# Kernel tuning notes

Hardware: AMD Instinct MI355X
Metric: run time of the kernel (lower is better)

The kernel has to match this reference:

```python
import jax, jax.numpy as jnp
import numpy as np
from jax import lax

# IVF+PQ search (FAISS IVF1024,PQ8x8 with nprobe=32, by_residual=False variant):
# 1) coarse quantizer: L2 distance of each query to nlist centroids, keep top nprobe lists
# 2) ADC: per-query LUT of squared distances between query subvectors and PQ codebooks,
#    database distance = sum over subquantizers of LUT gathered at the stored codes
# 3) mask database vectors whose IVF list was not probed, return indices of top_k smallest

NPROBE = 32  # top_n_centroids
BIG = jnp.float32(1e30)


def setup_inputs() -> dict:
    key = jax.random.key(0)
    ks = jax.random.split(key, 5)
    Q, D = 256, 128
    M, K = 8, 256          # pq_subvecs, 2**pq_nbits
    dsub = D // M          # 16
    nlist = 1024
    N = 250_000            # database size
    queries = jax.random.normal(ks[0], (Q, D), dtype=jnp.float32)
    centroids = jax.random.normal(ks[1], (nlist, D), dtype=jnp.float32)
    codebooks = jax.random.normal(ks[2], (M, K, dsub), dtype=jnp.float32)
    db_codes = jax.random.randint(ks[3], (N, M), 0, K, dtype=jnp.int32)
    db_list = jax.random.randint(ks[4], (N,), 0, nlist, dtype=jnp.int32)
    return {"queries": queries, "centroids": centroids, "codebooks": codebooks,
            "db_codes": db_codes, "db_list": db_list, "top_k": 100}


def _masked_adc_distances(queries, centroids, codebooks, db_codes, db_list):
    Q, D = queries.shape
    nlist = centroids.shape[0]
    M, K, dsub = codebooks.shape
    # ---- coarse quantizer: ||q - c||^2 over [Q, nlist] ----
    coarse = (jnp.sum(queries * queries, -1, keepdims=True)
              + jnp.sum(centroids * centroids, -1)[None, :]
              - 2.0 * queries @ centroids.T)
    _, probed = lax.top_k(-coarse, NPROBE)                      # [Q, NPROBE] list ids
    probe_mask = jnp.zeros((Q, nlist), dtype=bool).at[
        jnp.arange(Q)[:, None], probed].set(True)               # [Q, nlist]
    allowed = probe_mask[:, db_list]                            # [Q, N]
    # ---- PQ ADC lookup table: ||q_sub - codeword||^2, [Q, M, K] ----
    qs = queries.reshape(Q, M, dsub)
    lut = (jnp.sum(qs * qs, -1)[:, :, None]
           + jnp.sum(codebooks * codebooks, -1)[None, :, :]
           - 2.0 * jnp.einsum('qmd,mkd->qmk', qs, codebooks))   # [Q, M, K]
    # ---- accumulate gathered LUT entries over subquantizers ----
    dist = lut[:, 0, db_codes[:, 0]]                            # [Q, N]
    for m in range(1, M):
        dist = dist + lut[:, m, db_codes[:, m]]
    return jnp.where(allowed, dist, BIG)


def reference(queries, centroids, codebooks, db_codes, db_list, top_k):
    dist = _masked_adc_distances(queries, centroids, codebooks, db_codes, db_list)
    _, indices = lax.top_k(-dist, top_k)                        # smallest distances
    return indices
```

## Files before the change

### kernel.cpp

```cpp
#include <hip/hip_runtime.h>

#define DDIM 128
#define MSUB 8
#define KCODE 256
#define DSUB 16
#define NLIST 1024
#define NPROBE 32
#define TOPK 100
#define HBINS 4096
#define COLL_CAP 2048
#define RCAP 10
#define SCHUNK 1024


__device__ __forceinline__ float xla_sumsq128(const float* x) {
  float s[16];
  #pragma unroll
  for (int j = 0; j < 16; ++j) {
    float p0 = __fmul_rn(x[j],       x[j]);
    float p1 = __fmul_rn(x[j + 16],  x[j + 16]);
    float p2 = __fmul_rn(x[j + 32],  x[j + 32]);
    float p3 = __fmul_rn(x[j + 48],  x[j + 48]);
    float p4 = __fmul_rn(x[j + 64],  x[j + 64]);
    float p5 = __fmul_rn(x[j + 80],  x[j + 80]);
    float p6 = __fmul_rn(x[j + 96],  x[j + 96]);
    float p7 = __fmul_rn(x[j + 112], x[j + 112]);
    float r0 = __fadd_rn(p0, p4);
    float r1 = __fadd_rn(p1, p5);
    float r2 = __fadd_rn(p2, p6);
    float r3 = __fadd_rn(p3, p7);
    s[j] = __fadd_rn(__fadd_rn(r0, r1), __fadd_rn(r2, r3));
  }
  float a[8], b[4], c[2];
  #pragma unroll
  for (int j = 0; j < 8; ++j) a[j] = __fadd_rn(s[j], s[j + 8]);
  #pragma unroll
  for (int j = 0; j < 4; ++j) b[j] = __fadd_rn(a[j], a[j + 4]);
  #pragma unroll
  for (int j = 0; j < 2; ++j) c[j] = __fadd_rn(b[j], b[j + 2]);
  return __fadd_rn(c[0], c[1]);
}

__device__ __forceinline__ float xla_sumsq16(const float* x) {
  float p[16];
  #pragma unroll
  for (int j = 0; j < 16; ++j) p[j] = __fmul_rn(x[j], x[j]);
  float s8[8], s4[4], s2[2];
  #pragma unroll
  for (int j = 0; j < 8; ++j) s8[j] = __fadd_rn(p[j], p[j + 8]);
  #pragma unroll
  for (int j = 0; j < 4; ++j) s4[j] = __fadd_rn(s8[j], s8[j + 4]);
  #pragma unroll
  for (int j = 0; j < 2; ++j) s2[j] = __fadd_rn(s4[j], s4[j + 2]);
  return __fadd_rn(s2[0], s2[1]);
}

__device__ __forceinline__ float chain_dot16(const float* a, const float* b) {
  float dot = 0.f;
  #pragma unroll
  for (int d = 0; d < DSUB; ++d) dot = __fmaf_rn(a[d], b[d], dot);
  return dot;
}

__device__ __forceinline__ float adc_dist(const float* lut, unsigned long long code) {
  float d = lut[(unsigned)(code & 255ULL)];
  d = __fadd_rn(d, lut[256  + (unsigned)((code >> 8)  & 255ULL)]);
  d = __fadd_rn(d, lut[512  + (unsigned)((code >> 16) & 255ULL)]);
  d = __fadd_rn(d, lut[768  + (unsigned)((code >> 24) & 255ULL)]);
  d = __fadd_rn(d, lut[1024 + (unsigned)((code >> 32) & 255ULL)]);
  d = __fadd_rn(d, lut[1280 + (unsigned)((code >> 40) & 255ULL)]);
  d = __fadd_rn(d, lut[1536 + (unsigned)((code >> 48) & 255ULL)]);
  d = __fadd_rn(d, lut[1792 + (unsigned)((code >> 56) & 255ULL)]);
  return d;
}

__device__ __forceinline__ unsigned block_scan_incl(unsigned v, volatile unsigned* wsum,
                                                    int t, int nwaves) {
  int lane = t & 63, wid = t >> 6;
  #pragma unroll
  for (int off = 1; off < 64; off <<= 1) {
    unsigned u = __shfl_up(v, off, 64);
    if (lane >= off) v += u;
  }
  if (lane == 63) wsum[wid] = v;
  __syncthreads();
  if (wid == 0 && lane < nwaves) {
    unsigned wv = wsum[lane];
    #pragma unroll
    for (int off = 1; off < 16; off <<= 1) {
      unsigned u = __shfl_up(wv, off, 64);
      if (lane >= off) wv += u;
    }
    wsum[lane] = wv;
  }
  __syncthreads();
  return v + (wid > 0 ? wsum[wid - 1] : 0u);
}

__global__ __launch_bounds__(256) void k_coarse(const float* __restrict__ queries,
                                                const float* __restrict__ centroids,
                                                unsigned long long* __restrict__ keys_g) {
  const int qi = blockIdx.x >> 2;
  const int part = blockIdx.x & 3;
  const int t = threadIdx.x;
  __shared__ float qs[DDIM];
  if (t < DDIM) qs[t] = queries[qi * DDIM + t];
  __syncthreads();
  const float qq = xla_sumsq128(qs);
  const int c = part * 256 + t;
  const float* cr = centroids + (size_t)c * DDIM;
  float cbuf[DDIM];
  #pragma unroll
  for (int d = 0; d < DDIM; d += 4) {
    float4 cv = *(const float4*)(cr + d);
    cbuf[d] = cv.x; cbuf[d + 1] = cv.y; cbuf[d + 2] = cv.z; cbuf[d + 3] = cv.w;
  }
  const float cc = xla_sumsq128(cbuf);
  float dot = 0.f;
  #pragma unroll
  for (int d = 0; d < DDIM; ++d) dot = __fmaf_rn(qs[d], cbuf[d], dot);
  float dist = __fsub_rn(__fadd_rn(qq, cc), __fmul_rn(2.0f, dot));
  unsigned bits = __float_as_uint(dist);
  keys_g[(size_t)qi * NLIST + c] = ((unsigned long long)bits << 32) | (unsigned)c;
}

__global__ __launch_bounds__(256) void k_lut(const float* __restrict__ queries,
                                             const float* __restrict__ codebooks,
                                             const int* __restrict__ db_list, int N,
                                             float* __restrict__ lut_g,
                                             unsigned* __restrict__ counts) {
  const int qi = blockIdx.x;
  const int t = threadIdx.x;
  __shared__ float qs[DDIM];
  __shared__ unsigned hist[NLIST];
  if (t < DDIM) qs[t] = queries[qi * DDIM + t];
  for (int i = t; i < NLIST; i += 256) hist[i] = 0;
  __syncthreads();

  for (int j = 0; j < MSUB; ++j) {
    int idx = j * KCODE + t;
    const float* cb = codebooks + (size_t)idx * DSUB;
    const float* qsub = qs + j * DSUB;
    float cbv[DSUB], qv[DSUB];
    #pragma unroll
    for (int d = 0; d < DSUB; ++d) { cbv[d] = cb[d]; qv[d] = qsub[d]; }
    const float qq16 = xla_sumsq16(qv);
    const float cc16 = xla_sumsq16(cbv);
    const float dot16 = chain_dot16(qv, cbv);
    lut_g[(size_t)qi * (MSUB * KCODE) + idx] =
        __fsub_rn(__fadd_rn(qq16, cc16), __fmul_rn(2.0f, dot16));
  }

  for (int n = qi * 256 + t; n < N; n += 256 * 256)
    atomicAdd(&hist[db_list[n]], 1u);
  __syncthreads();
  for (int i = t; i < NLIST; i += 256)
    if (hist[i]) atomicAdd(&counts[i], hist[i]);
}

__global__ __launch_bounds__(256) void k_scatter(const int* __restrict__ db_list,
                                                 const int* __restrict__ db_codes, int N,
                                                 const unsigned* __restrict__ counts,
                                                 unsigned* __restrict__ cursor,
                                                 int4* __restrict__ pack) {
  __shared__ unsigned lhist[NLIST], lbase[NLIST], sbstart[NLIST];
  __shared__ unsigned wsum[16];
  const int t = threadIdx.x;
  const int base = blockIdx.x * SCHUNK;
  {
    unsigned c0 = counts[t * 4], c1 = counts[t * 4 + 1],
             c2 = counts[t * 4 + 2], c3 = counts[t * 4 + 3];
    unsigned sum4 = c0 + c1 + c2 + c3;
    unsigned incl = block_scan_incl(sum4, wsum, t, 4);
    unsigned excl = incl - sum4;
    sbstart[t * 4] = excl;
    sbstart[t * 4 + 1] = excl + c0;
    sbstart[t * 4 + 2] = excl + c0 + c1;
    sbstart[t * 4 + 3] = excl + c0 + c1 + c2;
  }
  for (int i = t; i < NLIST; i += 256) lhist[i] = 0;
  __syncthreads();
  #pragma unroll
  for (int k = 0; k < SCHUNK / 256; ++k) {
    int n = base + k * 256 + t;
    if (n < N) atomicAdd(&lhist[db_list[n]], 1u);
  }
  __syncthreads();
  for (int i = t; i < NLIST; i += 256) {
    unsigned cnt = lhist[i];
    if (cnt) lbase[i] = sbstart[i] + atomicAdd(&cursor[i], cnt);
    lhist[i] = 0;
  }
  __syncthreads();
  #pragma unroll
  for (int k = 0; k < SCHUNK / 256; ++k) {
    int n = base + k * 256 + t;
    if (n < N) {
      int l = db_list[n];
      unsigned pos = lbase[l] + atomicAdd(&lhist[l], 1u);
      const int4* cp = (const int4*)(db_codes + (size_t)n * MSUB);
      int4 c0 = cp[0], c1 = cp[1];
      unsigned lo = (unsigned)(c0.x & 255) | ((unsigned)(c0.y & 255) << 8) |
                    ((unsigned)(c0.z & 255) << 16) | ((unsigned)(c0.w & 255) << 24);
      unsigned hi = (unsigned)(c1.x & 255) | ((unsigned)(c1.y & 255) << 8) |
                    ((unsigned)(c1.z & 255) << 16) | ((unsigned)(c1.w & 255) << 24);
      pack[pos] = make_int4((int)lo, (int)hi, n, 0);
    }
  }
}

__global__ __launch_bounds__(1024, 1) void k_search(const float* __restrict__ lut_g,
                                                    const unsigned long long* __restrict__ keys_g,
                                                    const unsigned* __restrict__ counts,
                                                    const int4* __restrict__ pack,
                                                    int* __restrict__ out) {
  const int qi = blockIdx.x;
  const int t = threadIdx.x;
  __shared__ float lut_s[MSUB * KCODE];
  __shared__ unsigned hist[HBINS];
  __shared__ unsigned long long coll[COLL_CAP];
  __shared__ unsigned bst[NLIST + 1];
  __shared__ unsigned pstart[NPROBE], pcum[NPROBE + 1];
  __shared__ unsigned wsum[16];
  __shared__ unsigned scnt;
  __shared__ int sT;

  for (int i = t; i < MSUB * KCODE; i += 1024) lut_s[i] = lut_g[(size_t)qi * (MSUB * KCODE) + i];
  const unsigned long long ckey = keys_g[(size_t)qi * NLIST + t];
  for (int i = t; i < HBINS; i += 1024) hist[i] = 0;
  if (t == 0) { scnt = 0; sT = HBINS - 1; }
  {
    unsigned v = counts[t];
    unsigned incl = block_scan_incl(v, wsum, t, 16);
    bst[t + 1] = incl;
    if (t == 0) bst[0] = 0;
  }
  __syncthreads();

  atomicAdd(&hist[(unsigned)(ckey >> 51)], 1u);
  __syncthreads();
  {
    unsigned mysum = 0;
    #pragma unroll
    for (int i = 0; i < 4; ++i) mysum += hist[t * 4 + i];
    unsigned incl = block_scan_incl(mysum, wsum, t, 16);
    unsigned excl = incl - mysum;
    if (excl < NPROBE && NPROBE <= incl) {
      unsigned c2 = excl;
      #pragma unroll
      for (int i = 0; i < 4; ++i) {
        unsigned h = hist[t * 4 + i];
        if (c2 + h >= NPROBE) { sT = t * 4 + i; break; }
        c2 += h;
      }
    }
  }
  __syncthreads();
  {
    const int T32 = sT;
    if ((int)(ckey >> 51) <= T32) {
      unsigned p = atomicAdd(&scnt, 1u);
      if (p < 512) coll[p] = ckey;
    }
  }
  __syncthreads();
  {
    unsigned cnt = scnt; if (cnt > 512) cnt = 512;
    for (unsigned i = t; i < cnt; i += 1024) {
      unsigned long long k2 = coll[i];
      unsigned r = 0;
      for (unsigned j = 0; j < cnt; ++j) r += (coll[j] < k2) ? 1u : 0u;
      if (r < NPROBE) {
        unsigned l = (unsigned)(k2 & 0xffffffffULL);
        pstart[r] = bst[l];
        pcum[r + 1] = bst[l + 1] - bst[l];
      }
    }
  }
  __syncthreads();
  for (int i = t; i < HBINS; i += 1024) hist[i] = 0;
  if (t == 0) {
    scnt = 0; sT = HBINS - 1;
    unsigned acc = 0;
    pcum[0] = 0;
    for (int j = 1; j <= NPROBE; ++j) { acc += pcum[j]; pcum[j] = acc; }
  }
  __syncthreads();
  const unsigned total = pcum[NPROBE];

  unsigned regbits[RCAP], regaddr[RCAP];
  {
    int s = 0;
    for (unsigned g = t; g < total; g += 1024, ++s) {
      int lo = 0, hi = NPROBE;
      while (hi - lo > 1) { int mid = (lo + hi) >> 1; if (pcum[mid] <= g) lo = mid; else hi = mid; }
      unsigned addr = pstart[lo] + (g - pcum[lo]);
      int4 w = pack[addr];
      unsigned long long code = (unsigned)w.x | ((unsigned long long)(unsigned)w.y << 32);
      unsigned bits = __float_as_uint(adc_dist(lut_s, code));
      if (s < RCAP) { regbits[s] = bits; regaddr[s] = addr; }
      atomicAdd(&hist[bits >> 19], 1u);
    }
  }
  __syncthreads();

  {
    unsigned mysum = 0;
    #pragma unroll
    for (int i = 0; i < 4; ++i) mysum += hist[t * 4 + i];
    unsigned incl = block_scan_incl(mysum, wsum, t, 16);
    unsigned excl = incl - mysum;
    if (excl < TOPK && TOPK <= incl) {
      unsigned c = excl;
      #pragma unroll
      for (int i = 0; i < 4; ++i) {
        unsigned h = hist[t * 4 + i];
        if (c + h >= TOPK) { sT = t * 4 + i; break; }
        c += h;
      }
    }
  }
  __syncthreads();
  const int T = sT;

  {
    int s = 0;
    for (unsigned g = t; g < total; g += 1024, ++s) {
      unsigned bits, addr;
      if (s < RCAP) { bits = regbits[s]; addr = regaddr[s]; }
      else {
        int l2 = 0, hi = NPROBE;
        while (hi - l2 > 1) { int mid = (l2 + hi) >> 1; if (pcum[mid] <= g) l2 = mid; else hi = mid; }
        addr = pstart[l2] + (g - pcum[l2]);
        int4 w = pack[addr];
        unsigned long long code = (unsigned)w.x | ((unsigned long long)(unsigned)w.y << 32);
        bits = __float_as_uint(adc_dist(lut_s, code));
      }
      if ((int)(bits >> 19) <= T) {
        unsigned n = (unsigned)pack[addr].z;
        unsigned p = atomicAdd(&scnt, 1u);
        if (p < COLL_CAP) coll[p] = ((unsigned long long)bits << 32) | n;
      }
    }
  }
  __syncthreads();

  unsigned cnt = scnt;
  if (cnt > COLL_CAP) cnt = COLL_CAP;
  for (unsigned i = t; i < cnt; i += 1024) {
    unsigned long long key = coll[i];
    unsigned r = 0;
    for (unsigned j = 0; j < cnt; ++j) r += (coll[j] < key) ? 1u : 0u;
    if (r < TOPK) out[qi * TOPK + r] = (int)(key & 0xffffffffULL);
  }
}

extern "C" void kernel_launch(void* const* d_in, const int* in_sizes, int n_in,
                              void* d_out, int out_size, void* d_ws, size_t ws_size,
                              hipStream_t stream) {
  const float* queries   = (const float*)d_in[0];
  const float* centroids = (const float*)d_in[1];
  const float* codebooks = (const float*)d_in[2];
  const int*   db_codes  = (const int*)d_in[3];
  const int*   db_list   = (const int*)d_in[4];
  const int N = in_sizes[4];
  const int Q = in_sizes[0] / DDIM;
  int* out = (int*)d_out;

  char* p = (char*)d_ws;
  float* lut_g = (float*)p;                         p += (size_t)Q * MSUB * KCODE * 4;
  unsigned long long* keys_g = (unsigned long long*)p; p += (size_t)Q * NLIST * 8;
  unsigned* counts = (unsigned*)p;                  p += NLIST * 4;
  unsigned* cursor = (unsigned*)p;                  p += NLIST * 4;
  int4* pack = (int4*)p;                            p += (size_t)N * 16;

  hipMemsetAsync(counts, 0, (size_t)NLIST * 4 * 2, stream);

  k_coarse<<<Q * 4, 256, 0, stream>>>(queries, centroids, keys_g);
  k_lut<<<Q, 256, 0, stream>>>(queries, codebooks, db_list, N, lut_g, counts);
  k_scatter<<<(N + SCHUNK - 1) / SCHUNK, 256, 0, stream>>>(db_list, db_codes, N,
                                                           counts, cursor, pack);
  k_search<<<Q, 1024, 0, stream>>>(lut_g, keys_g, counts, pack, out);
}
```

Measured before the change: 132.7 us.

## Fuse coarse quantizer and LUT build into search kernel with 512-thread blocks

Coarse centroid distances and the PQ lookup table are now computed per query inside the search kernel, straight into shared memory. This removes the global round trips for keys and LUT and two kernel launches, leaving a small standalone histogram kernel. The search block drops to 512 threads with two blocks per CU, replaces per-element binary searches over probe offsets with a monotone linear walk, and caches packed keys (distance plus index) in registers (RCAP 18). The cost is that each block redoes 1024 centroid dot products serially, and register pressure is higher.

```diff
diff --git a/kernel.cpp b/kernel.cpp
--- a/kernel.cpp
+++ b/kernel.cpp
@@ -9,8 +9,9 @@
 #define TOPK 100
 #define HBINS 4096
 #define COLL_CAP 2048
-#define RCAP 10
+#define RCAP 18
 #define SCHUNK 1024
+#define FTHREADS 512
 
 
 __device__ __forceinline__ float xla_sumsq128(const float* x) {
@@ -97,61 +98,13 @@
   return v + (wid > 0 ? wsum[wid - 1] : 0u);
 }
 
-__global__ __launch_bounds__(256) void k_coarse(const float* __restrict__ queries,
-                                                const float* __restrict__ centroids,
-                                                unsigned long long* __restrict__ keys_g) {
-  const int qi = blockIdx.x >> 2;
-  const int part = blockIdx.x & 3;
+__global__ __launch_bounds__(256) void k_hist(const int* __restrict__ db_list, int N,
+                                              unsigned* __restrict__ counts) {
+  __shared__ unsigned hist[NLIST];
   const int t = threadIdx.x;
-  __shared__ float qs[DDIM];
-  if (t < DDIM) qs[t] = queries[qi * DDIM + t];
-  __syncthreads();
-  const float qq = xla_sumsq128(qs);
-  const int c = part * 256 + t;
-  const float* cr = centroids + (size_t)c * DDIM;
-  float cbuf[DDIM];
-  #pragma unroll
-  for (int d = 0; d < DDIM; d += 4) {
-    float4 cv = *(const float4*)(cr + d);
-    cbuf[d] = cv.x; cbuf[d + 1] = cv.y; cbuf[d + 2] = cv.z; cbuf[d + 3] = cv.w;
-  }
-  const float cc = xla_sumsq128(cbuf);
-  float dot = 0.f;
-  #pragma unroll
-  for (int d = 0; d < DDIM; ++d) dot = __fmaf_rn(qs[d], cbuf[d], dot);
-  float dist = __fsub_rn(__fadd_rn(qq, cc), __fmul_rn(2.0f, dot));
-  unsigned bits = __float_as_uint(dist);
-  keys_g[(size_t)qi * NLIST + c] = ((unsigned long long)bits << 32) | (unsigned)c;
-}
-
-__global__ __launch_bounds__(256) void k_lut(const float* __restrict__ queries,
-                                             const float* __restrict__ codebooks,
-                                             const int* __restrict__ db_list, int N,
-                                             float* __restrict__ lut_g,
-                                             unsigned* __restrict__ counts) {
-  const int qi = blockIdx.x;
-  const int t = threadIdx.x;
-  __shared__ float qs[DDIM];
-  __shared__ unsigned hist[NLIST];
-  if (t < DDIM) qs[t] = queries[qi * DDIM + t];
   for (int i = t; i < NLIST; i += 256) hist[i] = 0;
   __syncthreads();
-
-  for (int j = 0; j < MSUB; ++j) {
-    int idx = j * KCODE + t;
-    const float* cb = codebooks + (size_t)idx * DSUB;
-    const float* qsub = qs + j * DSUB;
-    float cbv[DSUB], qv[DSUB];
-    #pragma unroll
-    for (int d = 0; d < DSUB; ++d) { cbv[d] = cb[d]; qv[d] = qsub[d]; }
-    const float qq16 = xla_sumsq16(qv);
-    const float cc16 = xla_sumsq16(cbv);
-    const float dot16 = chain_dot16(qv, cbv);
-    lut_g[(size_t)qi * (MSUB * KCODE) + idx] =
-        __fsub_rn(__fadd_rn(qq16, cc16), __fmul_rn(2.0f, dot16));
-  }
-
-  for (int n = qi * 256 + t; n < N; n += 256 * 256)
+  for (int n = blockIdx.x * 256 + t; n < N; n += 256 * 256)
     atomicAdd(&hist[db_list[n]], 1u);
   __syncthreads();
   for (int i = t; i < NLIST; i += 256)
@@ -209,14 +162,17 @@
   }
 }
 
-__global__ __launch_bounds__(1024, 1) void k_search(const float* __restrict__ lut_g,
-                                                    const unsigned long long* __restrict__ keys_g,
-                                                    const unsigned* __restrict__ counts,
-                                                    const int4* __restrict__ pack,
-                                                    int* __restrict__ out) {
+__global__ __launch_bounds__(FTHREADS, 2) void k_fused(const float* __restrict__ queries,
+                                                       const float* __restrict__ centroids,
+                                                       const float* __restrict__ codebooks,
+                                                       const unsigned* __restrict__ counts,
+                                                       const int4* __restrict__ pack,
+                                                       int* __restrict__ out) {
   const int qi = blockIdx.x;
   const int t = threadIdx.x;
+  __shared__ float qs[DDIM];
   __shared__ float lut_s[MSUB * KCODE];
+  __shared__ unsigned long long keys_s[NLIST];
   __shared__ unsigned hist[HBINS];
   __shared__ unsigned long long coll[COLL_CAP];
   __shared__ unsigned bst[NLIST + 1];
@@ -225,32 +181,69 @@
   __shared__ unsigned scnt;
   __shared__ int sT;
 
-  for (int i = t; i < MSUB * KCODE; i += 1024) lut_s[i] = lut_g[(size_t)qi * (MSUB * KCODE) + i];
-  const unsigned long long ckey = keys_g[(size_t)qi * NLIST + t];
-  for (int i = t; i < HBINS; i += 1024) hist[i] = 0;
+  if (t < DDIM) qs[t] = queries[qi * DDIM + t];
+  for (int i = t; i < HBINS; i += FTHREADS) hist[i] = 0;
   if (t == 0) { scnt = 0; sT = HBINS - 1; }
-  {
-    unsigned v = counts[t];
-    unsigned incl = block_scan_incl(v, wsum, t, 16);
-    bst[t + 1] = incl;
+  __syncthreads();
+
+  const float qq = xla_sumsq128(qs);
+  #pragma unroll 1
+  for (int rep = 0; rep < 2; ++rep) {
+    const int c = rep * FTHREADS + t;
+    const float* cr = centroids + (size_t)c * DDIM;
+    float cbuf[DDIM];
+    #pragma unroll
+    for (int d = 0; d < DDIM; d += 4) {
+      float4 cv = *(const float4*)(cr + d);
+      cbuf[d] = cv.x; cbuf[d + 1] = cv.y; cbuf[d + 2] = cv.z; cbuf[d + 3] = cv.w;
+    }
+    const float cc = xla_sumsq128(cbuf);
+    float dot = 0.f;
+    #pragma unroll
+    for (int d = 0; d < DDIM; ++d) dot = __fmaf_rn(qs[d], cbuf[d], dot);
+    float dist = __fsub_rn(__fadd_rn(qq, cc), __fmul_rn(2.0f, dot));
+    unsigned bits = __float_as_uint(dist);
+    keys_s[c] = ((unsigned long long)bits << 32) | (unsigned)c;
+    atomicAdd(&hist[bits >> 19], 1u);
+  }
+
+  #pragma unroll 1
+  for (int j = 0; j < (MSUB * KCODE) / FTHREADS; ++j) {
+    int idx = j * FTHREADS + t;
+    const float* cb = codebooks + (size_t)idx * DSUB;
+    const float* qsub = qs + (idx >> 8) * DSUB;
+    float cbv[DSUB], qv[DSUB];
+    #pragma unroll
+    for (int d = 0; d < DSUB; ++d) { cbv[d] = cb[d]; qv[d] = qsub[d]; }
+    const float qq16 = xla_sumsq16(qv);
+    const float cc16 = xla_sumsq16(cbv);
+    const float dot16 = chain_dot16(qv, cbv);
+    lut_s[idx] = __fsub_rn(__fadd_rn(qq16, cc16), __fmul_rn(2.0f, dot16));
+  }
+  __syncthreads();
+
+  {
+    unsigned c0 = counts[2 * t], c1 = counts[2 * t + 1];
+    unsigned s2 = c0 + c1;
+    unsigned incl = block_scan_incl(s2, wsum, t, FTHREADS / 64);
+    bst[2 * t + 1] = incl - c1;
+    bst[2 * t + 2] = incl;
     if (t == 0) bst[0] = 0;
   }
   __syncthreads();
 
-  atomicAdd(&hist[(unsigned)(ckey >> 51)], 1u);
-  __syncthreads();
   {
     unsigned mysum = 0;
     #pragma unroll
-    for (int i = 0; i < 4; ++i) mysum += hist[t * 4 + i];
-    unsigned incl = block_scan_incl(mysum, wsum, t, 16);
+    for (int i = 0; i < HBINS / FTHREADS; ++i) mysum += hist[t * (HBINS / FTHREADS) + i];
+    unsigned incl = block_scan_incl(mysum, wsum, t, FTHREADS / 64);
     unsigned excl = incl - mysum;
     if (excl < NPROBE && NPROBE <= incl) {
       unsigned c2 = excl;
       #pragma unroll
-      for (int i = 0; i < 4; ++i) {
-        unsigned h = hist[t * 4 + i];
-        if (c2 + h >= NPROBE) { sT = t * 4 + i; break; }
+      for (int i = 0; i < HBINS / FTHREADS; ++i) {
+        unsigned h = hist[t * (HBINS / FTHREADS) + i];
+        if (c2 + h >= NPROBE) { sT = t * (HBINS / FTHREADS) + i; break; }
         c2 += h;
       }
     }
@@ -258,15 +251,18 @@
   __syncthreads();
   {
     const int T32 = sT;
-    if ((int)(ckey >> 51) <= T32) {
-      unsigned p = atomicAdd(&scnt, 1u);
-      if (p < 512) coll[p] = ckey;
+    for (int c = t; c < NLIST; c += FTHREADS) {
+      unsigned long long k2 = keys_s[c];
+      if ((int)(unsigned)(k2 >> 51) <= T32) {
+        unsigned p = atomicAdd(&scnt, 1u);
+        if (p < 512) coll[p] = k2;
+      }
     }
   }
   __syncthreads();
   {
     unsigned cnt = scnt; if (cnt > 512) cnt = 512;
-    for (unsigned i = t; i < cnt; i += 1024) {
+    for (unsigned i = t; i < cnt; i += FTHREADS) {
       unsigned long long k2 = coll[i];
       unsigned r = 0;
       for (unsigned j = 0; j < cnt; ++j) r += (coll[j] < k2) ? 1u : 0u;
@@ -278,7 +274,7 @@
     }
   }
   __syncthreads();
-  for (int i = t; i < HBINS; i += 1024) hist[i] = 0;
+  for (int i = t; i < HBINS; i += FTHREADS) hist[i] = 0;
   if (t == 0) {
     scnt = 0; sT = HBINS - 1;
     unsigned acc = 0;
@@ -288,34 +284,43 @@
   __syncthreads();
   const unsigned total = pcum[NPROBE];
 
-  unsigned regbits[RCAP], regaddr[RCAP];
-  {
-    int s = 0;
-    for (unsigned g = t; g < total; g += 1024, ++s) {
-      int lo = 0, hi = NPROBE;
-      while (hi - lo > 1) { int mid = (lo + hi) >> 1; if (pcum[mid] <= g) lo = mid; else hi = mid; }
+  unsigned long long regkey[RCAP];
+  int lo = 0;
+  #pragma unroll
+  for (int s = 0; s < RCAP; ++s) {
+    unsigned g = (unsigned)t + (unsigned)(s * FTHREADS);
+    if (g < total) {
+      while (pcum[lo + 1] <= g) ++lo;
       unsigned addr = pstart[lo] + (g - pcum[lo]);
       int4 w = pack[addr];
       unsigned long long code = (unsigned)w.x | ((unsigned long long)(unsigned)w.y << 32);
       unsigned bits = __float_as_uint(adc_dist(lut_s, code));
-      if (s < RCAP) { regbits[s] = bits; regaddr[s] = addr; }
+      regkey[s] = ((unsigned long long)bits << 32) | (unsigned)w.z;
       atomicAdd(&hist[bits >> 19], 1u);
     }
   }
+  for (unsigned g = (unsigned)t + RCAP * FTHREADS; g < total; g += FTHREADS) {
+    while (pcum[lo + 1] <= g) ++lo;
+    unsigned addr = pstart[lo] + (g - pcum[lo]);
+    int4 w = pack[addr];
+    unsigned long long code = (unsigned)w.x | ((unsigned long long)(unsigned)w.y << 32);
+    unsigned bits = __float_as_uint(adc_dist(lut_s, code));
+    atomicAdd(&hist[bits >> 19], 1u);
+  }
   __syncthreads();
 
   {
     unsigned mysum = 0;
     #pragma unroll
-    for (int i = 0; i < 4; ++i) mysum += hist[t * 4 + i];
-    unsigned incl = block_scan_incl(mysum, wsum, t, 16);
+    for (int i = 0; i < HBINS / FTHREADS; ++i) mysum += hist[t * (HBINS / FTHREADS) + i];
+    unsigned incl = block_scan_incl(mysum, wsum, t, FTHREADS / 64);
     unsigned excl = incl - mysum;
     if (excl < TOPK && TOPK <= incl) {
       unsigned c = excl;
       #pragma unroll
-      for (int i = 0; i < 4; ++i) {
-        unsigned h = hist[t * 4 + i];
-        if (c + h >= TOPK) { sT = t * 4 + i; break; }
+      for (int i = 0; i < HBINS / FTHREADS; ++i) {
+        unsigned h = hist[t * (HBINS / FTHREADS) + i];
+        if (c + h >= TOPK) { sT = t * (HBINS / FTHREADS) + i; break; }
         c += h;
       }
     }
@@ -324,22 +329,27 @@
   const int T = sT;
 
   {
-    int s = 0;
-    for (unsigned g = t; g < total; g += 1024, ++s) {
-      unsigned bits, addr;
-      if (s < RCAP) { bits = regbits[s]; addr = regaddr[s]; }
-      else {
-        int l2 = 0, hi = NPROBE;
-        while (hi - l2 > 1) { int mid = (l2 + hi) >> 1; if (pcum[mid] <= g) l2 = mid; else hi = mid; }
-        addr = pstart[l2] + (g - pcum[l2]);
-        int4 w = pack[addr];
-        unsigned long long code = (unsigned)w.x | ((unsigned long long)(unsigned)w.y << 32);
-        bits = __float_as_uint(adc_dist(lut_s, code));
-      }
+    #pragma unroll
+    for (int s = 0; s < RCAP; ++s) {
+      unsigned g = (unsigned)t + (unsigned)(s * FTHREADS);
+      if (g < total) {
+        unsigned long long k2 = regkey[s];
+        if ((int)(unsigned)(k2 >> 51) <= T) {
+          unsigned p = atomicAdd(&scnt, 1u);
+          if (p < COLL_CAP) coll[p] = k2;
+        }
+      }
+    }
+    int lo2 = 0;
+    for (unsigned g = (unsigned)t + RCAP * FTHREADS; g < total; g += FTHREADS) {
+      while (pcum[lo2 + 1] <= g) ++lo2;
+      unsigned addr = pstart[lo2] + (g - pcum[lo2]);
+      int4 w = pack[addr];
+      unsigned long long code = (unsigned)w.x | ((unsigned long long)(unsigned)w.y << 32);
+      unsigned bits = __float_as_uint(adc_dist(lut_s, code));
       if ((int)(bits >> 19) <= T) {
-        unsigned n = (unsigned)pack[addr].z;
         unsigned p = atomicAdd(&scnt, 1u);
-        if (p < COLL_CAP) coll[p] = ((unsigned long long)bits << 32) | n;
+        if (p < COLL_CAP) coll[p] = ((unsigned long long)bits << 32) | (unsigned)w.z;
       }
     }
   }
@@ -347,7 +357,7 @@
 
   unsigned cnt = scnt;
   if (cnt > COLL_CAP) cnt = COLL_CAP;
-  for (unsigned i = t; i < cnt; i += 1024) {
+  for (unsigned i = t; i < cnt; i += FTHREADS) {
     unsigned long long key = coll[i];
     unsigned r = 0;
     for (unsigned j = 0; j < cnt; ++j) r += (coll[j] < key) ? 1u : 0u;
@@ -368,17 +378,14 @@
   int* out = (int*)d_out;
 
   char* p = (char*)d_ws;
-  float* lut_g = (float*)p;                         p += (size_t)Q * MSUB * KCODE * 4;
-  unsigned long long* keys_g = (unsigned long long*)p; p += (size_t)Q * NLIST * 8;
   unsigned* counts = (unsigned*)p;                  p += NLIST * 4;
   unsigned* cursor = (unsigned*)p;                  p += NLIST * 4;
   int4* pack = (int4*)p;                            p += (size_t)N * 16;
 
   hipMemsetAsync(counts, 0, (size_t)NLIST * 4 * 2, stream);
 
-  k_coarse<<<Q * 4, 256, 0, stream>>>(queries, centroids, keys_g);
-  k_lut<<<Q, 256, 0, stream>>>(queries, codebooks, db_list, N, lut_g, counts);
+  k_hist<<<256, 256, 0, stream>>>(db_list, N, counts);
   k_scatter<<<(N + SCHUNK - 1) / SCHUNK, 256, 0, stream>>>(db_list, db_codes, N,
                                                            counts, cursor, pack);
-  k_search<<<Q, 1024, 0, stream>>>(lut_g, keys_g, counts, pack, out);
-}
+  k_fused<<<Q, FTHREADS, 0, stream>>>(queries, centroids, codebooks, counts, pack, out);
+}
```

Result: slower. 138.5 us (+4.3%).

## Fuse LUT computation into search kernel and store full keys in registers

Applied to the files above, without the earlier changes.

Moves the per-query PQ lookup-table computation from the separate k_lut kernel into k_search, building it directly in shared memory and dropping the global LUT buffer and its round trip. k_lut becomes a plain histogram kernel. The search loop now keeps the full (distance, index) key in registers, so the collection pass no longer re-reads pack entries. The per-element binary search over probe offsets is replaced by a monotonic linear advance. In exchange, every search block recomputes its LUT from codebooks (8 entries per thread), and holding 64-bit keys raises register pressure.

```diff
diff --git a/kernel.cpp b/kernel.cpp
--- a/kernel.cpp
+++ b/kernel.cpp
@@ -124,34 +124,13 @@
   keys_g[(size_t)qi * NLIST + c] = ((unsigned long long)bits << 32) | (unsigned)c;
 }
 
-__global__ __launch_bounds__(256) void k_lut(const float* __restrict__ queries,
-                                             const float* __restrict__ codebooks,
-                                             const int* __restrict__ db_list, int N,
-                                             float* __restrict__ lut_g,
-                                             unsigned* __restrict__ counts) {
-  const int qi = blockIdx.x;
+__global__ __launch_bounds__(256) void k_hist(const int* __restrict__ db_list, int N,
+                                              unsigned* __restrict__ counts) {
+  __shared__ unsigned hist[NLIST];
   const int t = threadIdx.x;
-  __shared__ float qs[DDIM];
-  __shared__ unsigned hist[NLIST];
-  if (t < DDIM) qs[t] = queries[qi * DDIM + t];
   for (int i = t; i < NLIST; i += 256) hist[i] = 0;
   __syncthreads();
-
-  for (int j = 0; j < MSUB; ++j) {
-    int idx = j * KCODE + t;
-    const float* cb = codebooks + (size_t)idx * DSUB;
-    const float* qsub = qs + j * DSUB;
-    float cbv[DSUB], qv[DSUB];
-    #pragma unroll
-    for (int d = 0; d < DSUB; ++d) { cbv[d] = cb[d]; qv[d] = qsub[d]; }
-    const float qq16 = xla_sumsq16(qv);
-    const float cc16 = xla_sumsq16(cbv);
-    const float dot16 = chain_dot16(qv, cbv);
-    lut_g[(size_t)qi * (MSUB * KCODE) + idx] =
-        __fsub_rn(__fadd_rn(qq16, cc16), __fmul_rn(2.0f, dot16));
-  }
-
-  for (int n = qi * 256 + t; n < N; n += 256 * 256)
+  for (int n = blockIdx.x * 256 + t; n < N; n += 256 * 256)
     atomicAdd(&hist[db_list[n]], 1u);
   __syncthreads();
   for (int i = t; i < NLIST; i += 256)
@@ -209,13 +188,15 @@
   }
 }
 
-__global__ __launch_bounds__(1024, 1) void k_search(const float* __restrict__ lut_g,
+__global__ __launch_bounds__(1024, 1) void k_search(const float* __restrict__ queries,
+                                                    const float* __restrict__ codebooks,
                                                     const unsigned long long* __restrict__ keys_g,
                                                     const unsigned* __restrict__ counts,
                                                     const int4* __restrict__ pack,
                                                     int* __restrict__ out) {
   const int qi = blockIdx.x;
   const int t = threadIdx.x;
+  __shared__ float qs[DDIM];
   __shared__ float lut_s[MSUB * KCODE];
   __shared__ unsigned hist[HBINS];
   __shared__ unsigned long long coll[COLL_CAP];
@@ -225,7 +206,7 @@
   __shared__ unsigned scnt;
   __shared__ int sT;
 
-  for (int i = t; i < MSUB * KCODE; i += 1024) lut_s[i] = lut_g[(size_t)qi * (MSUB * KCODE) + i];
+  if (t < DDIM) qs[t] = queries[qi * DDIM + t];
   const unsigned long long ckey = keys_g[(size_t)qi * NLIST + t];
   for (int i = t; i < HBINS; i += 1024) hist[i] = 0;
   if (t == 0) { scnt = 0; sT = HBINS - 1; }
@@ -236,6 +217,20 @@
     if (t == 0) bst[0] = 0;
   }
   __syncthreads();
+
+  #pragma unroll
+  for (int j = 0; j < (MSUB * KCODE) / 1024; ++j) {
+    int idx = j * 1024 + t;
+    const float* cb = codebooks + (size_t)idx * DSUB;
+    const float* qsub = qs + (idx >> 8) * DSUB;
+    float cbv[DSUB], qv[DSUB];
+    #pragma unroll
+    for (int d = 0; d < DSUB; ++d) { cbv[d] = cb[d]; qv[d] = qsub[d]; }
+    const float qq16 = xla_sumsq16(qv);
+    const float cc16 = xla_sumsq16(cbv);
+    const float dot16 = chain_dot16(qv, cbv);
+    lut_s[idx] = __fsub_rn(__fadd_rn(qq16, cc16), __fmul_rn(2.0f, dot16));
+  }
 
   atomicAdd(&hist[(unsigned)(ckey >> 51)], 1u);
   __syncthreads();
@@ -288,19 +283,28 @@
   __syncthreads();
   const unsigned total = pcum[NPROBE];
 
-  unsigned regbits[RCAP], regaddr[RCAP];
-  {
-    int s = 0;
-    for (unsigned g = t; g < total; g += 1024, ++s) {
-      int lo = 0, hi = NPROBE;
-      while (hi - lo > 1) { int mid = (lo + hi) >> 1; if (pcum[mid] <= g) lo = mid; else hi = mid; }
+  unsigned long long regkey[RCAP];
+  int lo = 0;
+  #pragma unroll
+  for (int s = 0; s < RCAP; ++s) {
+    unsigned g = (unsigned)t + (unsigned)(s * 1024);
+    if (g < total) {
+      while (pcum[lo + 1] <= g) ++lo;
       unsigned addr = pstart[lo] + (g - pcum[lo]);
       int4 w = pack[addr];
       unsigned long long code = (unsigned)w.x | ((unsigned long long)(unsigned)w.y << 32);
       unsigned bits = __float_as_uint(adc_dist(lut_s, code));
-      if (s < RCAP) { regbits[s] = bits; regaddr[s] = addr; }
+      regkey[s] = ((unsigned long long)bits << 32) | (unsigned)w.z;
       atomicAdd(&hist[bits >> 19], 1u);
     }
+  }
+  for (unsigned g = (unsigned)t + RCAP * 1024; g < total; g += 1024) {
+    while (pcum[lo + 1] <= g) ++lo;
+    unsigned addr = pstart[lo] + (g - pcum[lo]);
+    int4 w = pack[addr];
+    unsigned long long code = (unsigned)w.x | ((unsigned long long)(unsigned)w.y << 32);
+    unsigned bits = __float_as_uint(adc_dist(lut_s, code));
+    atomicAdd(&hist[bits >> 19], 1u);
   }
   __syncthreads();
 
@@ -324,22 +328,27 @@
   const int T = sT;
 
   {
-    int s = 0;
-    for (unsigned g = t; g < total; g += 1024, ++s) {
-      unsigned bits, addr;
-      if (s < RCAP) { bits = regbits[s]; addr = regaddr[s]; }
-      else {
-        int l2 = 0, hi = NPROBE;
-        while (hi - l2 > 1) { int mid = (l2 + hi) >> 1; if (pcum[mid] <= g) l2 = mid; else hi = mid; }
-        addr = pstart[l2] + (g - pcum[l2]);
-        int4 w = pack[addr];
-        unsigned long long code = (unsigned)w.x | ((unsigned long long)(unsigned)w.y << 32);
-        bits = __float_as_uint(adc_dist(lut_s, code));
-      }
+    #pragma unroll
+    for (int s = 0; s < RCAP; ++s) {
+      unsigned g = (unsigned)t + (unsigned)(s * 1024);
+      if (g < total) {
+        unsigned long long k2 = regkey[s];
+        if ((int)(unsigned)(k2 >> 51) <= T) {
+          unsigned p = atomicAdd(&scnt, 1u);
+          if (p < COLL_CAP) coll[p] = k2;
+        }
+      }
+    }
+    int lo2 = 0;
+    for (unsigned g = (unsigned)t + RCAP * 1024; g < total; g += 1024) {
+      while (pcum[lo2 + 1] <= g) ++lo2;
+      unsigned addr = pstart[lo2] + (g - pcum[lo2]);
+      int4 w = pack[addr];
+      unsigned long long code = (unsigned)w.x | ((unsigned long long)(unsigned)w.y << 32);
+      unsigned bits = __float_as_uint(adc_dist(lut_s, code));
       if ((int)(bits >> 19) <= T) {
-        unsigned n = (unsigned)pack[addr].z;
         unsigned p = atomicAdd(&scnt, 1u);
-        if (p < COLL_CAP) coll[p] = ((unsigned long long)bits << 32) | n;
+        if (p < COLL_CAP) coll[p] = ((unsigned long long)bits << 32) | (unsigned)w.z;
       }
     }
   }
@@ -368,7 +377,6 @@
   int* out = (int*)d_out;
 
   char* p = (char*)d_ws;
-  float* lut_g = (float*)p;                         p += (size_t)Q * MSUB * KCODE * 4;
   unsigned long long* keys_g = (unsigned long long*)p; p += (size_t)Q * NLIST * 8;
   unsigned* counts = (unsigned*)p;                  p += NLIST * 4;
   unsigned* cursor = (unsigned*)p;                  p += NLIST * 4;
@@ -377,8 +385,8 @@
   hipMemsetAsync(counts, 0, (size_t)NLIST * 4 * 2, stream);
 
   k_coarse<<<Q * 4, 256, 0, stream>>>(queries, centroids, keys_g);
-  k_lut<<<Q, 256, 0, stream>>>(queries, codebooks, db_list, N, lut_g, counts);
+  k_hist<<<256, 256, 0, stream>>>(db_list, N, counts);
   k_scatter<<<(N + SCHUNK - 1) / SCHUNK, 256, 0, stream>>>(db_list, db_codes, N,
                                                            counts, cursor, pack);
-  k_search<<<Q, 1024, 0, stream>>>(lut_g, keys_g, counts, pack, out);
-}
+  k_search<<<Q, 1024, 0, stream>>>(queries, codebooks, keys_g, counts, pack, out);
+}
```

Measured after the change: 129.8 us. -2.2%, faster.
